# Kernel optimization log

Measured on AMD Instinct MI355X. Metric: run time of the kernel, lower is better.

## Reference

```python
import jax, jax.numpy as jnp
import numpy as np

NEG_INF = -jnp.inf


def setup_inputs() -> dict:
    key = jax.random.key(0)
    ks = jax.random.split(key, 6)
    B, S, D, H, Dh = 2, 2048, 1024, 16, 64
    std = 0.02
    return {
        "x": jax.random.normal(ks[0], (B, S, D), dtype=jnp.float32),
        "W_Q": jax.random.normal(ks[1], (H, D, Dh), dtype=jnp.float32) * std,
        "W_K": jax.random.normal(ks[2], (H, D, Dh), dtype=jnp.float32) * std,
        "W_V": jax.random.normal(ks[3], (H, D, Dh), dtype=jnp.float32) * std,
        "W_O": jax.random.normal(ks[4], (H, Dh, D), dtype=jnp.float32) * std,
        "b_Q": jnp.zeros((H, Dh), dtype=jnp.float32),
        "b_K": jnp.zeros((H, Dh), dtype=jnp.float32),
        "b_V": jnp.zeros((H, Dh), dtype=jnp.float32),
        "b_O": jnp.zeros((D,), dtype=jnp.float32),
    }


def reference(x, W_Q, W_K, W_V, W_O, b_Q, b_K, b_V, b_O):
    # x: [B, S, D]; W_{Q,K,V}: [H, D, Dh]; W_O: [H, Dh, D]
    d_head = W_Q.shape[-1]
    q = jnp.einsum('bsd,hde->bshe', x, W_Q) + b_Q  # [B, S, H, Dh]
    k = jnp.einsum('bsd,hde->bshe', x, W_K) + b_K
    v = jnp.einsum('bsd,hde->bshe', x, W_V) + b_V
    # Attention scores: [B, H, S_q, S_k]
    scores = jnp.einsum('bqhe,bkhe->bhqk', q, k) / jnp.sqrt(jnp.float32(d_head))
    S = scores.shape[-1]
    causal = jnp.tril(jnp.ones((S, S), dtype=bool))  # True = keep
    scores = jnp.where(causal, scores, NEG_INF)
    pattern = jax.nn.softmax(scores, axis=-1)
    z = jnp.einsum('bhqk,bkhe->bqhe', pattern, v)  # [B, S, H, Dh]
    out = jnp.einsum('bqhe,hed->bqd', z, W_O) + b_O  # [B, S, D]
    return out
```

## Files before the change

kernel.cpp:

```cpp
#include <hip/hip_runtime.h>

typedef __attribute__((ext_vector_type(8))) short short8;
typedef __attribute__((ext_vector_type(4))) short short4_t;
typedef __attribute__((ext_vector_type(4))) float f32x4;
typedef __attribute__((ext_vector_type(4))) float float4_t;
typedef __attribute__((ext_vector_type(8))) __bf16 bf16x8;

#define MFMA16(a, b, c) __builtin_amdgcn_mfma_f32_16x16x32_bf16( \
    __builtin_bit_cast(bf16x8, a), __builtin_bit_cast(bf16x8, b), (c), 0, 0, 0)

__device__ __forceinline__ short f2bf(float f) {
    unsigned u = __builtin_bit_cast(unsigned, f);
    u += 0x7fffu + ((u >> 16) & 1u);
    return (short)(u >> 16);
}

__device__ __forceinline__ void gload16(const short* g, char* lds) {
    __builtin_amdgcn_global_load_lds(
        (const __attribute__((address_space(1))) unsigned int*)g,
        (__attribute__((address_space(3))) unsigned int*)lds, 16, 0, 0);
}

#define BB 2
#define SS 2048
#define DD 1024
#define HH 16
#define DH 64
#define MM (BB * SS)

__global__ __launch_bounds__(256) void prep_x(const float* __restrict__ x, short* __restrict__ xb) {
    int c = blockIdx.x * 256 + threadIdx.x;
    float4_t v = *reinterpret_cast<const float4_t*>(x + (size_t)c * 4);
    short4_t s;
    s[0] = f2bf(v[0]); s[1] = f2bf(v[1]); s[2] = f2bf(v[2]); s[3] = f2bf(v[3]);
    *reinterpret_cast<short4_t*>(xb + (size_t)c * 4) = s;
}

__global__ __launch_bounds__(256) void trans_qkvw(
    const float* __restrict__ wq, const float* __restrict__ wk, const float* __restrict__ wv,
    short* __restrict__ dst)
{
    const int z = blockIdx.y;
    const int t = z >> 4, h = z & 15;
    const float* src = (t == 0 ? wq : (t == 1 ? wk : wv)) + (size_t)h * DD * DH;
    short* d = dst + (size_t)z * DD * DH;
    const int r0 = blockIdx.x * 64;
    __shared__ float tle[64][65];
    const int tid = threadIdx.x;
    {
        int rr = tid >> 4, c4 = (tid & 15) * 4;
        #pragma unroll
        for (int i = 0; i < 4; ++i) {
            float4_t v = *reinterpret_cast<const float4_t*>(src + (size_t)(r0 + rr + i * 16) * DH + c4);
            tle[rr + i * 16][c4] = v[0]; tle[rr + i * 16][c4 + 1] = v[1];
            tle[rr + i * 16][c4 + 2] = v[2]; tle[rr + i * 16][c4 + 3] = v[3];
        }
    }
    __syncthreads();
    {
        int cc = tid >> 2, r16 = (tid & 3) * 16;
        short8 o0, o1;
        #pragma unroll
        for (int j = 0; j < 8; ++j) o0[j] = f2bf(tle[r16 + j][cc]);
        #pragma unroll
        for (int j = 0; j < 8; ++j) o1[j] = f2bf(tle[r16 + 8 + j][cc]);
        *reinterpret_cast<short8*>(d + (size_t)cc * DD + r0 + r16)     = o0;
        *reinterpret_cast<short8*>(d + (size_t)cc * DD + r0 + r16 + 8) = o1;
    }
}

__global__ __launch_bounds__(256) void trans64(const float* __restrict__ src, short* __restrict__ dst,
                                               int R, int C) {
    const int c0 = blockIdx.x * 64, r0 = blockIdx.y * 64;
    __shared__ float t[64][65];
    const int tid = threadIdx.x;
    {
        int rr = tid >> 4, c4 = (tid & 15) * 4;
        #pragma unroll
        for (int i = 0; i < 4; ++i) {
            float4_t v = *reinterpret_cast<const float4_t*>(src + (size_t)(r0 + rr + i * 16) * C + c0 + c4);
            t[rr + i * 16][c4] = v[0]; t[rr + i * 16][c4 + 1] = v[1];
            t[rr + i * 16][c4 + 2] = v[2]; t[rr + i * 16][c4 + 3] = v[3];
        }
    }
    __syncthreads();
    {
        int cc = tid >> 2, r16 = (tid & 3) * 16;
        short8 o0, o1;
        #pragma unroll
        for (int j = 0; j < 8; ++j) o0[j] = f2bf(t[r16 + j][cc]);
        #pragma unroll
        for (int j = 0; j < 8; ++j) o1[j] = f2bf(t[r16 + 8 + j][cc]);
        *reinterpret_cast<short8*>(dst + (size_t)(c0 + cc) * R + r0 + r16)     = o0;
        *reinterpret_cast<short8*>(dst + (size_t)(c0 + cc) * R + r0 + r16 + 8) = o1;
    }
}

__global__ __launch_bounds__(256) void qkv_gemm(
    const short* __restrict__ xb, const short* __restrict__ wt,
    const float* __restrict__ bq, const float* __restrict__ bk, const float* __restrict__ bv,
    short* __restrict__ q, short* __restrict__ k, short* __restrict__ vtg)
{
    const int tid = threadIdx.x;
    const int rowbase = blockIdx.x * 128;
    const int th = blockIdx.y;
    const int t = th >> 4, h = th & 15;
    const short* wth = wt + (size_t)th * DH * DD;

    __shared__ short As[128 * 64];
    __shared__ short Bs[64 * 64];
    char* Ab = (char*)As;
    char* Bb = (char*)Bs;

    const int lane = tid & 63;
    const int wid  = tid >> 6;
    const int wrow = wid * 32;

    f32x4 acc[2][4] = {};

    for (int k0 = 0; k0 < DD; k0 += 64) {
        #pragma unroll
        for (int i = 0; i < 4; ++i) {
            int b = i * 4096 + tid * 16;
            int row = b >> 7;
            int colb = (b & 127) ^ ((row & 7) << 4);
            gload16(xb + (size_t)(rowbase + row) * DD + k0 + (colb >> 1), Ab + b);
        }
        #pragma unroll
        for (int i = 0; i < 2; ++i) {
            int b = i * 4096 + tid * 16;
            int n = b >> 7;
            int kb_ = (b & 127) ^ ((n & 7) << 4);
            gload16(wth + (size_t)n * DD + k0 + (kb_ >> 1), Bb + b);
        }
        __syncthreads();

        #pragma unroll
        for (int kk = 0; kk < 2; ++kk) {
            int ko = (kk * 32 + (lane >> 4) * 8) * 2;
            short8 a[2], bfr[4];
            #pragma unroll
            for (int rb = 0; rb < 2; ++rb) {
                int ar = wrow + rb * 16 + (lane & 15);
                a[rb] = *reinterpret_cast<short8*>(Ab + ((ar * 128 + ko) ^ ((ar & 7) << 4)));
            }
            #pragma unroll
            for (int cb = 0; cb < 4; ++cb) {
                int bc = cb * 16 + (lane & 15);
                bfr[cb] = *reinterpret_cast<short8*>(Bb + ((bc * 128 + ko) ^ ((bc & 7) << 4)));
            }
            #pragma unroll
            for (int rb = 0; rb < 2; ++rb)
                #pragma unroll
                for (int cb = 0; cb < 4; ++cb)
                    acc[rb][cb] = MFMA16(a[rb], bfr[cb], acc[rb][cb]);
        }
        __syncthreads();
    }

    const float* biasp = (t == 0 ? bq : (t == 1 ? bk : bv)) + h * DH;
    #pragma unroll
    for (int cb = 0; cb < 4; ++cb) {
        int dh = cb * 16 + (lane & 15);
        float bval = biasp[dh];
        if (t < 2) {
            short* outp = (t == 0 ? q : k);
            #pragma unroll
            for (int rb = 0; rb < 2; ++rb) {
                #pragma unroll
                for (int r = 0; r < 4; ++r) {
                    int grow = rowbase + wrow + rb * 16 + (lane >> 4) * 4 + r;
                    int b_ = grow >> 11, s_ = grow & (SS - 1);
                    outp[(((size_t)(b_ * HH + h)) * SS + s_) * DH + dh] = f2bf(acc[rb][cb][r] + bval);
                }
            }
        } else {
            #pragma unroll
            for (int rb = 0; rb < 2; ++rb) {
                int grow0 = rowbase + wrow + rb * 16 + (lane >> 4) * 4;
                int b_ = grow0 >> 11, s0 = grow0 & (SS - 1);
                short4_t s4;
                #pragma unroll
                for (int r = 0; r < 4; ++r) s4[r] = f2bf(acc[rb][cb][r] + bval);
                *reinterpret_cast<short4_t*>(vtg + (((size_t)(b_ * HH + h)) * DH + dh) * SS + s0) = s4;
            }
        }
    }
}

__global__ __launch_bounds__(256, 4) void attn_kernel(
    const short* __restrict__ qg, const short* __restrict__ kg, const short* __restrict__ vtg,
    short* __restrict__ zg)
{
    const int tid  = threadIdx.x;
    const int lane = tid & 63;
    const int w    = tid >> 6;

    const int gid = blockIdx.x;
    const int bh = gid & 31;
    const int pr = gid >> 5;
    const int b = bh >> 4, h = bh & 15;

    const short* qh  = qg  + (size_t)bh * SS * DH;
    const short* kh  = kg  + (size_t)bh * SS * DH;
    const short* vth = vtg + (size_t)bh * DH * SS;

    const float SCL = 0.125f * 1.44269504088896f;
    const float NC  = -24.0f * SCL;
    const float NEGINF = -__builtin_inff();

    __shared__ short Ks[2][64 * 64];
    __shared__ short Vts[2][64 * 64];
    __shared__ short Ps[4][16 * 64];
    char* Pb = (char*)(Ps[w]);

    short8 ones;
    #pragma unroll
    for (int j = 0; j < 8; ++j) ones[j] = (short)0x3F80;

    auto STAGE = [&](int buf, int kbase) {
        char* Kb = (char*)(Ks[buf]); char* Vb = (char*)(Vts[buf]);
        #pragma unroll
        for (int i = 0; i < 2; ++i) {
            int b_2 = i * 4096 + tid * 16;
            int row = b_2 >> 7;
            int db_ = (b_2 & 127) ^ ((row & 7) << 4);
            gload16(kh + (size_t)(kbase + row) * DH + (db_ >> 1), Kb + b_2);
        }
        #pragma unroll
        for (int i = 0; i < 2; ++i) {
            int b_2 = i * 4096 + tid * 16;
            int dh = b_2 >> 7;
            int kvb = (b_2 & 127) ^ ((dh & 7) << 4);
            gload16(vth + (size_t)dh * SS + kbase + (kvb >> 1), Vb + b_2);
        }
    };

    STAGE(0, 0);
    __syncthreads();
    int cur = 0;

    for (int seg = 0; seg < 2; ++seg) {
        const int qt = (seg == 0) ? (31 - pr) : pr;
        const int qbase = qt * 64;

        short8 qf[2];
        {
            int qr = qbase + w * 16 + (lane & 15);
            #pragma unroll
            for (int kk = 0; kk < 2; ++kk)
                qf[kk] = *reinterpret_cast<const short8*>(qh + (size_t)qr * DH + kk * 32 + (lane >> 4) * 8);
        }

        f32x4 o[4] = {};
        f32x4 lacc = {};

        for (int kt = 0; kt <= qt; ++kt) {
            const int kbase = kt * 64;
            if (kt < qt) STAGE(cur ^ 1, kbase + 64);
            else if (seg == 0) STAGE(cur ^ 1, 0);
            char* Kb = (char*)(Ks[cur]); char* Vb = (char*)(Vts[cur]);

            f32x4 sfr[4] = {};
            #pragma unroll
            for (int kk = 0; kk < 2; ++kk) {
                int ko = (kk * 32 + (lane >> 4) * 8) * 2;
                __builtin_amdgcn_s_setprio(1);
                #pragma unroll
                for (int cb = 0; cb < 4; ++cb) {
                    int kc = cb * 16 + (lane & 15);
                    short8 kf = *reinterpret_cast<short8*>(Kb + ((kc * 128 + ko) ^ ((kc & 7) << 4)));
                    sfr[cb] = MFMA16(kf, qf[kk], sfr[cb]);
                }
                __builtin_amdgcn_s_setprio(0);
            }

            if (kt == qt) {
                int qrg = qbase + w * 16 + (lane & 15);
                #pragma unroll
                for (int cb = 0; cb < 4; ++cb) {
                    #pragma unroll
                    for (int r = 0; r < 4; ++r) {
                        int kcg = kbase + cb * 16 + (lane >> 4) * 4 + r;
                        if (kcg > qrg) sfr[cb][r] = NEGINF;
                    }
                }
            }

            {
                int q_ = lane & 15;
                int rowb = q_ * 128;
                int sw = (q_ & 7) << 4;
                #pragma unroll
                for (int cb = 0; cb < 4; ++cb) {
                    short4_t s4;
                    #pragma unroll
                    for (int r = 0; r < 4; ++r)
                        s4[r] = f2bf(__builtin_amdgcn_exp2f(fmaf(sfr[cb][r], SCL, NC)));
                    int off = (rowb + cb * 32 + (lane >> 4) * 8) ^ sw;
                    *reinterpret_cast<short4_t*>(Pb + off) = s4;
                }
            }

            #pragma unroll
            for (int kk = 0; kk < 2; ++kk) {
                int ko = (kk * 32 + (lane >> 4) * 8) * 2;
                int ar = (lane & 15);
                short8 pa = *reinterpret_cast<short8*>(Pb + ((ar * 128 + ko) ^ ((ar & 7) << 4)));
                __builtin_amdgcn_s_setprio(1);
                lacc = MFMA16(pa, ones, lacc);
                #pragma unroll
                for (int db = 0; db < 4; ++db) {
                    int dh_ = db * 16 + (lane & 15);
                    short8 vf = *reinterpret_cast<short8*>(Vb + ((dh_ * 128 + ko) ^ ((dh_ & 7) << 4)));
                    o[db] = MFMA16(pa, vf, o[db]);
                }
                __builtin_amdgcn_s_setprio(0);
            }
            __syncthreads();
            cur ^= 1;
        }

        float rl[4];
        #pragma unroll
        for (int r = 0; r < 4; ++r) rl[r] = 1.0f / lacc[r];
        #pragma unroll
        for (int db = 0; db < 4; ++db) {
            #pragma unroll
            for (int r = 0; r < 4; ++r) {
                float val = o[db][r] * rl[r];
                int qr = qbase + w * 16 + (lane >> 4) * 4 + r;
                zg[((size_t)(b * SS + qr)) * DD + h * 64 + db * 16 + (lane & 15)] = f2bf(val);
            }
        }
    }
}

__global__ __launch_bounds__(256) void out_gemm(
    const short* __restrict__ z, const short* __restrict__ wot,
    const float* __restrict__ bo, float* __restrict__ out)
{
    const int tid = threadIdx.x;
    const int rowbase = blockIdx.x * 128;
    const int cbase   = blockIdx.y * 64;

    __shared__ short As[2][128 * 64];
    __shared__ short Bs[2][64 * 64];

    const int lane = tid & 63;
    const int wid  = tid >> 6;
    const int wrow = wid * 32;

    f32x4 acc[2][4] = {};

    auto STAGE = [&](int buf, int k0) {
        char* Ab = (char*)(As[buf]); char* Bb = (char*)(Bs[buf]);
        #pragma unroll
        for (int i = 0; i < 4; ++i) {
            int b = i * 4096 + tid * 16;
            int row = b >> 7;
            int colb = (b & 127) ^ ((row & 7) << 4);
            gload16(z + (size_t)(rowbase + row) * DD + k0 + (colb >> 1), Ab + b);
        }
        #pragma unroll
        for (int i = 0; i < 2; ++i) {
            int b = i * 4096 + tid * 16;
            int n = b >> 7;
            int kb_ = (b & 127) ^ ((n & 7) << 4);
            gload16(wot + (size_t)(cbase + n) * DD + k0 + (kb_ >> 1), Bb + b);
        }
    };

    STAGE(0, 0);
    __syncthreads();
    int cur = 0;

    for (int s = 0; s < 16; ++s) {
        if (s < 15) STAGE(cur ^ 1, (s + 1) * 64);
        char* Ab = (char*)(As[cur]); char* Bb = (char*)(Bs[cur]);

        #pragma unroll
        for (int kk = 0; kk < 2; ++kk) {
            int ko = (kk * 32 + (lane >> 4) * 8) * 2;
            short8 a[2], bfr[4];
            #pragma unroll
            for (int rb = 0; rb < 2; ++rb) {
                int ar = wrow + rb * 16 + (lane & 15);
                a[rb] = *reinterpret_cast<short8*>(Ab + ((ar * 128 + ko) ^ ((ar & 7) << 4)));
            }
            #pragma unroll
            for (int cb = 0; cb < 4; ++cb) {
                int bc = cb * 16 + (lane & 15);
                bfr[cb] = *reinterpret_cast<short8*>(Bb + ((bc * 128 + ko) ^ ((bc & 7) << 4)));
            }
            #pragma unroll
            for (int rb = 0; rb < 2; ++rb)
                #pragma unroll
                for (int cb = 0; cb < 4; ++cb)
                    acc[rb][cb] = MFMA16(a[rb], bfr[cb], acc[rb][cb]);
        }
        __syncthreads();
        cur ^= 1;
    }

    #pragma unroll
    for (int rb = 0; rb < 2; ++rb) {
        #pragma unroll
        for (int cb = 0; cb < 4; ++cb) {
            int col = cbase + cb * 16 + (lane & 15);
            float bv_ = bo[col];
            #pragma unroll
            for (int r = 0; r < 4; ++r) {
                int grow = rowbase + wrow + rb * 16 + (lane >> 4) * 4 + r;
                out[(size_t)grow * DD + col] = acc[rb][cb][r] + bv_;
            }
        }
    }
}

extern "C" void kernel_launch(void* const* d_in, const int* in_sizes, int n_in,
                              void* d_out, int out_size, void* d_ws, size_t ws_size,
                              hipStream_t stream) {
    const float* x  = (const float*)d_in[0];
    const float* wq = (const float*)d_in[1];
    const float* wk = (const float*)d_in[2];
    const float* wv = (const float*)d_in[3];
    const float* wo = (const float*)d_in[4];
    const float* bq = (const float*)d_in[5];
    const float* bk = (const float*)d_in[6];
    const float* bv = (const float*)d_in[7];
    const float* bo = (const float*)d_in[8];
    float* out = (float*)d_out;

    char* ws = (char*)d_ws;
    short* xb  = (short*)(ws);
    short* wt  = (short*)(ws + (8u  << 20));
    short* wot = (short*)(ws + (14u << 20));
    short* qb  = (short*)(ws + (16u << 20));
    short* kb  = (short*)(ws + (24u << 20));
    short* vtb = (short*)(ws + (32u << 20));
    short* zb  = (short*)(ws + (40u << 20));

    prep_x<<<MM * DD / 1024, 256, 0, stream>>>(x, xb);
    trans_qkvw<<<dim3(16, 48), 256, 0, stream>>>(wq, wk, wv, wt);
    trans64<<<dim3(16, 16), 256, 0, stream>>>(wo, wot, DD, DD);

    qkv_gemm<<<dim3(MM / 128, 48), 256, 0, stream>>>(xb, wt, bq, bk, bv, qb, kb, vtb);
    attn_kernel<<<dim3(512), 256, 0, stream>>>(qb, kb, vtb, zb);
    out_gemm<<<dim3(MM / 128, DD / 64), 256, 0, stream>>>(zb, wot, bo, out);
}
```

Measured before the change: 102.9 us.

## Use 128-row query tiles per attention block instead of paired 64-row segments

Each attention block now owns a single 128-row query tile, with each warp holding two 16-row MFMA fragments. Every staged 64-key K/V tile is therefore reused across twice as many query rows, halving the LDS K/V traffic per unit of work. The P scratch buffer grows, and launch bounds drop from 4 to 3 blocks per CU to fit the extra registers. This gives up the old scheme that paired a long and a short causal tile per block, so block run times now range from 2 to 32 key tiles. That imbalance, plus the lower occupancy, could offset the reuse gain.

After: 112.4 us. 1.09x slower.

```diff
diff --git a/kernel.cpp b/kernel.cpp
--- a/kernel.cpp
+++ b/kernel.cpp
@@ -188,7 +188,7 @@
     }
 }
 
-__global__ __launch_bounds__(256, 4) void attn_kernel(
+__global__ __launch_bounds__(256, 3) void attn_kernel(
     const short* __restrict__ qg, const short* __restrict__ kg, const short* __restrict__ vtg,
     short* __restrict__ zg)
 {
@@ -197,26 +197,39 @@
     const int w    = tid >> 6;
 
     const int gid = blockIdx.x;
+    const int qt = 15 - (gid >> 5);
     const int bh = gid & 31;
-    const int pr = gid >> 5;
     const int b = bh >> 4, h = bh & 15;
 
     const short* qh  = qg  + (size_t)bh * SS * DH;
     const short* kh  = kg  + (size_t)bh * SS * DH;
     const short* vth = vtg + (size_t)bh * DH * SS;
 
+    const int qbase = qt * 128;
     const float SCL = 0.125f * 1.44269504088896f;
     const float NC  = -24.0f * SCL;
     const float NEGINF = -__builtin_inff();
 
     __shared__ short Ks[2][64 * 64];
     __shared__ short Vts[2][64 * 64];
-    __shared__ short Ps[4][16 * 64];
+    __shared__ short Ps[4][32 * 64];
     char* Pb = (char*)(Ps[w]);
+
+    short8 qf[2][2];
+    #pragma unroll
+    for (int rb = 0; rb < 2; ++rb) {
+        int qr = qbase + w * 32 + rb * 16 + (lane & 15);
+        #pragma unroll
+        for (int kk = 0; kk < 2; ++kk)
+            qf[rb][kk] = *reinterpret_cast<const short8*>(qh + (size_t)qr * DH + kk * 32 + (lane >> 4) * 8);
+    }
 
     short8 ones;
     #pragma unroll
     for (int j = 0; j < 8; ++j) ones[j] = (short)0x3F80;
+
+    f32x4 o[2][4] = {};
+    f32x4 lacc[2] = {};
 
     auto STAGE = [&](int buf, int kbase) {
         char* Kb = (char*)(Ks[buf]); char* Vb = (char*)(Vts[buf]);
@@ -240,96 +253,94 @@
     __syncthreads();
     int cur = 0;
 
-    for (int seg = 0; seg < 2; ++seg) {
-        const int qt = (seg == 0) ? (31 - pr) : pr;
-        const int qbase = qt * 64;
-
-        short8 qf[2];
-        {
-            int qr = qbase + w * 16 + (lane & 15);
-            #pragma unroll
-            for (int kk = 0; kk < 2; ++kk)
-                qf[kk] = *reinterpret_cast<const short8*>(qh + (size_t)qr * DH + kk * 32 + (lane >> 4) * 8);
-        }
-
-        f32x4 o[4] = {};
-        f32x4 lacc = {};
-
-        for (int kt = 0; kt <= qt; ++kt) {
-            const int kbase = kt * 64;
-            if (kt < qt) STAGE(cur ^ 1, kbase + 64);
-            else if (seg == 0) STAGE(cur ^ 1, 0);
-            char* Kb = (char*)(Ks[cur]); char* Vb = (char*)(Vts[cur]);
-
-            f32x4 sfr[4] = {};
-            #pragma unroll
-            for (int kk = 0; kk < 2; ++kk) {
-                int ko = (kk * 32 + (lane >> 4) * 8) * 2;
-                __builtin_amdgcn_s_setprio(1);
-                #pragma unroll
-                for (int cb = 0; cb < 4; ++cb) {
-                    int kc = cb * 16 + (lane & 15);
-                    short8 kf = *reinterpret_cast<short8*>(Kb + ((kc * 128 + ko) ^ ((kc & 7) << 4)));
-                    sfr[cb] = MFMA16(kf, qf[kk], sfr[cb]);
-                }
-                __builtin_amdgcn_s_setprio(0);
-            }
-
-            if (kt == qt) {
-                int qrg = qbase + w * 16 + (lane & 15);
+    const int ktmax = 2 * qt + 1;
+    for (int kt = 0; kt <= ktmax; ++kt) {
+        const int kbase = kt * 64;
+        if (kt < ktmax) STAGE(cur ^ 1, kbase + 64);
+        char* Kb = (char*)(Ks[cur]); char* Vb = (char*)(Vts[cur]);
+
+        f32x4 sfr[2][4] = {};
+        #pragma unroll
+        for (int kk = 0; kk < 2; ++kk) {
+            int ko = (kk * 32 + (lane >> 4) * 8) * 2;
+            __builtin_amdgcn_s_setprio(1);
+            #pragma unroll
+            for (int cb = 0; cb < 4; ++cb) {
+                int kc = cb * 16 + (lane & 15);
+                short8 kf = *reinterpret_cast<short8*>(Kb + ((kc * 128 + ko) ^ ((kc & 7) << 4)));
+                sfr[0][cb] = MFMA16(kf, qf[0][kk], sfr[0][cb]);
+                sfr[1][cb] = MFMA16(kf, qf[1][kk], sfr[1][cb]);
+            }
+            __builtin_amdgcn_s_setprio(0);
+        }
+
+        if (kt >= 2 * qt) {
+            #pragma unroll
+            for (int rb = 0; rb < 2; ++rb) {
+                int qrg = qbase + w * 32 + rb * 16 + (lane & 15);
                 #pragma unroll
                 for (int cb = 0; cb < 4; ++cb) {
                     #pragma unroll
                     for (int r = 0; r < 4; ++r) {
                         int kcg = kbase + cb * 16 + (lane >> 4) * 4 + r;
-                        if (kcg > qrg) sfr[cb][r] = NEGINF;
+                        if (kcg > qrg) sfr[rb][cb][r] = NEGINF;
                     }
                 }
             }
-
-            {
-                int q_ = lane & 15;
-                int rowb = q_ * 128;
-                int sw = (q_ & 7) << 4;
-                #pragma unroll
-                for (int cb = 0; cb < 4; ++cb) {
-                    short4_t s4;
-                    #pragma unroll
-                    for (int r = 0; r < 4; ++r)
-                        s4[r] = f2bf(__builtin_amdgcn_exp2f(fmaf(sfr[cb][r], SCL, NC)));
-                    int off = (rowb + cb * 32 + (lane >> 4) * 8) ^ sw;
-                    *reinterpret_cast<short4_t*>(Pb + off) = s4;
-                }
-            }
-
-            #pragma unroll
-            for (int kk = 0; kk < 2; ++kk) {
-                int ko = (kk * 32 + (lane >> 4) * 8) * 2;
-                int ar = (lane & 15);
-                short8 pa = *reinterpret_cast<short8*>(Pb + ((ar * 128 + ko) ^ ((ar & 7) << 4)));
-                __builtin_amdgcn_s_setprio(1);
-                lacc = MFMA16(pa, ones, lacc);
-                #pragma unroll
-                for (int db = 0; db < 4; ++db) {
-                    int dh_ = db * 16 + (lane & 15);
-                    short8 vf = *reinterpret_cast<short8*>(Vb + ((dh_ * 128 + ko) ^ ((dh_ & 7) << 4)));
-                    o[db] = MFMA16(pa, vf, o[db]);
-                }
-                __builtin_amdgcn_s_setprio(0);
-            }
-            __syncthreads();
-            cur ^= 1;
-        }
-
+        }
+
+        #pragma unroll
+        for (int rb = 0; rb < 2; ++rb) {
+            int prow = rb * 16 + (lane & 15);
+            int rowb = prow * 128;
+            int sw = (prow & 7) << 4;
+            #pragma unroll
+            for (int cb = 0; cb < 4; ++cb) {
+                short4_t s4;
+                #pragma unroll
+                for (int r = 0; r < 4; ++r)
+                    s4[r] = f2bf(__builtin_amdgcn_exp2f(fmaf(sfr[rb][cb][r], SCL, NC)));
+                int off = (rowb + cb * 32 + (lane >> 4) * 8) ^ sw;
+                *reinterpret_cast<short4_t*>(Pb + off) = s4;
+            }
+        }
+
+        #pragma unroll
+        for (int kk = 0; kk < 2; ++kk) {
+            int ko = (kk * 32 + (lane >> 4) * 8) * 2;
+            short8 pa[2];
+            #pragma unroll
+            for (int rb = 0; rb < 2; ++rb) {
+                int ar = rb * 16 + (lane & 15);
+                pa[rb] = *reinterpret_cast<short8*>(Pb + ((ar * 128 + ko) ^ ((ar & 7) << 4)));
+            }
+            __builtin_amdgcn_s_setprio(1);
+            lacc[0] = MFMA16(pa[0], ones, lacc[0]);
+            lacc[1] = MFMA16(pa[1], ones, lacc[1]);
+            #pragma unroll
+            for (int db = 0; db < 4; ++db) {
+                int dh_ = db * 16 + (lane & 15);
+                short8 vf = *reinterpret_cast<short8*>(Vb + ((dh_ * 128 + ko) ^ ((dh_ & 7) << 4)));
+                o[0][db] = MFMA16(pa[0], vf, o[0][db]);
+                o[1][db] = MFMA16(pa[1], vf, o[1][db]);
+            }
+            __builtin_amdgcn_s_setprio(0);
+        }
+        __syncthreads();
+        cur ^= 1;
+    }
+
+    #pragma unroll
+    for (int rb = 0; rb < 2; ++rb) {
         float rl[4];
         #pragma unroll
-        for (int r = 0; r < 4; ++r) rl[r] = 1.0f / lacc[r];
+        for (int r = 0; r < 4; ++r) rl[r] = 1.0f / lacc[rb][r];
         #pragma unroll
         for (int db = 0; db < 4; ++db) {
             #pragma unroll
             for (int r = 0; r < 4; ++r) {
-                float val = o[db][r] * rl[r];
-                int qr = qbase + w * 16 + (lane >> 4) * 4 + r;
+                float val = o[rb][db][r] * rl[r];
+                int qr = qbase + w * 32 + rb * 16 + (lane >> 4) * 4 + r;
                 zg[((size_t)(b * SS + qr)) * DD + h * 64 + db * 16 + (lane & 15)] = f2bf(val);
             }
         }
```
